# Kernel optimization log

Measured on AMD Instinct MI355X. Metric: run time of the kernel, lower is better.

## Reference

```python
import jax, jax.numpy as jnp
import numpy as np

D_K = 64

def setup_inputs() -> dict:
    key = jax.random.key(0)
    kq, kk, kv = jax.random.split(key, 3)
    shape = (2, 16, 2048, D_K)  # [B, H, S, d_k]
    q = jax.random.normal(kq, shape, dtype=jnp.float32)
    k = jax.random.normal(kk, shape, dtype=jnp.float32)
    v = jax.random.normal(kv, shape, dtype=jnp.float32)
    return {"q": q, "k": k, "v": v}

def reference(q, k, v):
    # score = q @ k^T / sqrt(d_k)  -> [B, H, S, S]
    scale = 1.0 / np.sqrt(D_K).astype(np.float32)
    score = jnp.einsum("bhqd,bhkd->bhqk", q, k) * scale
    attn = jax.nn.softmax(score, axis=-1)
    # dropout is identity in eval mode
    out = jnp.einsum("bhqk,bhkd->bhqd", attn, v)
    return out
```

## Files before the change

### kernel.cpp

```cpp
#include <hip/hip_runtime.h>
#include <hip/hip_bf16.h>
#include <math.h>
#include <stdint.h>


#define S_LEN 2048
#define DK 64
#define QW 32
#define NW 4
#define QBLK (QW * NW)
#define KVBLK 64
#define NT (S_LEN / KVBLK)
#define LOG2E 1.44269504088896340736f
#define THR 8.0f

typedef __attribute__((ext_vector_type(16))) float f32x16;
typedef __attribute__((ext_vector_type(8)))  __bf16 bf16x8;
typedef __attribute__((ext_vector_type(4)))  __bf16 bf16x4;
typedef __attribute__((ext_vector_type(4)))  uint32_t u32x4;

union frag_cast { u32x4 u; bf16x8 h; };

__device__ __forceinline__ uint32_t cvt_pk_bf16(float lo, float hi) {
    uint32_t r;
    asm("v_cvt_pk_bf16_f32 %0, %1, %2" : "=v"(r) : "v"(lo), "v"(hi));
    return r;
}
__device__ __forceinline__ void perm32swap(uint32_t& a, uint32_t& b) {
    asm volatile("v_permlane32_swap_b32 %0, %1" : "+v"(a), "+v"(b));
}
__device__ __forceinline__ void load_lds16(const __bf16* g, __bf16* l) {
    __builtin_amdgcn_global_load_lds(
        (const __attribute__((address_space(1))) void*)g,
        (__attribute__((address_space(3))) void*)l, 16, 0, 0);
}
__device__ __forceinline__ bf16x8 pack8(float4 a, float4 b) {
    bf16x8 f;
    f[0] = (__bf16)a.x; f[1] = (__bf16)a.y; f[2] = (__bf16)a.z; f[3] = (__bf16)a.w;
    f[4] = (__bf16)b.x; f[5] = (__bf16)b.y; f[6] = (__bf16)b.z; f[7] = (__bf16)b.w;
    return f;
}

__global__ __launch_bounds__(256)
void prep_pack(const float* __restrict__ Kg, const float* __restrict__ Vg,
               __bf16* __restrict__ Kimg, __bf16* __restrict__ Vimg)
{
    __shared__ float Vs[64 * 65];
    const int tid = threadIdx.x;
    const int t = blockIdx.x, bh = blockIdx.y;
    const size_t ibase = ((size_t)bh * S_LEN + (size_t)t * 64) * DK;
    const size_t obase = ((size_t)bh * NT + t) * 4096;

    #pragma unroll
    for (int u0 = 0; u0 < 2; ++u0) {
        const int u = tid + 256 * u0;
        const int f = u >> 6, lane = u & 63;
        const int sp = f >> 1, kt2 = f & 1;
        const int row = kt2 * 32 + (lane & 31);
        const int col = 16 * sp + 8 * (lane >> 5);
        const float* src = Kg + ibase + row * 64 + col;
        float4 a = *(const float4*)(src);
        float4 b = *(const float4*)(src + 4);
        *(bf16x8*)(Kimg + obase + (size_t)u * 8) = pack8(a, b);
    }

    {
        const int r = tid >> 2, c0 = (tid & 3) * 16;
        const float* src = Vg + ibase + r * 64 + c0;
        #pragma unroll
        for (int m = 0; m < 4; ++m) {
            float4 x = *(const float4*)(src + 4 * m);
            float* dst = &Vs[r * 65 + c0 + 4 * m];
            dst[0] = x.x; dst[1] = x.y; dst[2] = x.z; dst[3] = x.w;
        }
    }
    __syncthreads();
    #pragma unroll
    for (int u0 = 0; u0 < 2; ++u0) {
        const int u = tid + 256 * u0;
        const int g = u >> 6, lane = u & 63;
        const int ks = g >> 1, dt = g & 1;
        const int k0 = 16 * ks + 8 * (lane >> 5);
        const int d  = dt * 32 + (lane & 31);
        bf16x8 wv;
        #pragma unroll
        for (int i = 0; i < 8; ++i) wv[i] = (__bf16)Vs[(k0 + i) * 65 + d];
        *(bf16x8*)(Vimg + obase + (size_t)u * 8) = wv;
    }
}

__global__ __launch_bounds__(256, 2)
void attn_fwd_lds(const float* __restrict__ Qg, const __bf16* __restrict__ Kimg,
                  const __bf16* __restrict__ Vimg, float* __restrict__ Og)
{
    __shared__ __align__(16) __bf16 Kl[2][4096];
    __shared__ __align__(16) __bf16 Vt[2][4096];

    const int tid = threadIdx.x;
    const int lane = tid & 63;
    const int w   = tid >> 6;
    const int l31 = lane & 31;
    const int hi  = lane >> 5;

    const int qt = blockIdx.x;
    const int bh = blockIdx.y;
    const size_t base = (size_t)bh * (S_LEN * DK);
    const int q0g = qt * QBLK + w * QW;

    bf16x8 qf[4];
    {
        const float sc = 0.125f * LOG2E;
        const float* qrow = Qg + base + (size_t)(q0g + l31) * DK;
        #pragma unroll
        for (int sp = 0; sp < 4; ++sp) {
            const int d0 = 16 * sp + 8 * hi;
            float4 a = *(const float4*)(qrow + d0);
            float4 b = *(const float4*)(qrow + d0 + 4);
            bf16x8 f;
            f[0] = (__bf16)(a.x * sc); f[1] = (__bf16)(a.y * sc);
            f[2] = (__bf16)(a.z * sc); f[3] = (__bf16)(a.w * sc);
            f[4] = (__bf16)(b.x * sc); f[5] = (__bf16)(b.y * sc);
            f[6] = (__bf16)(b.z * sc); f[7] = (__bf16)(b.w * sc);
            qf[sp] = f;
        }
    }

    bf16x8 ones;
    #pragma unroll
    for (int i = 0; i < 8; ++i) ones[i] = (__bf16)1.0f;

    f32x16 acc0 = {}, acc1 = {}, acc2 = {};
    float m_run = -INFINITY;

    const __bf16* kbase = Kimg + (size_t)bh * NT * 4096;
    const __bf16* vbase = Vimg + (size_t)bh * NT * 4096;
    const int loff = lane * 8;

    auto stage = [&](int t, int b) {
        const __bf16* kt = kbase + (size_t)t * 4096 + tid * 8;
        const __bf16* vt = vbase + (size_t)t * 4096 + tid * 8;
        load_lds16(kt,        &Kl[b][w * 512]);
        load_lds16(kt + 2048, &Kl[b][2048 + w * 512]);
        load_lds16(vt,        &Vt[b][w * 512]);
        load_lds16(vt + 2048, &Vt[b][2048 + w * 512]);
    };

    stage(0, 0);
    __syncthreads();

    int cur = 0;
    #pragma unroll 1
    for (int t = 0; t < NT; ++t) {
        if (t + 1 < NT) stage(t + 1, cur ^ 1);

        f32x16 s0 = {}, s1 = {};
        __builtin_amdgcn_s_setprio(1);
        #pragma unroll
        for (int sp = 0; sp < 4; ++sp) {
            bf16x8 kb0 = *(const bf16x8*)(&Kl[cur][(sp * 2 + 0) * 512 + loff]);
            bf16x8 kb1 = *(const bf16x8*)(&Kl[cur][(sp * 2 + 1) * 512 + loff]);
            s0 = __builtin_amdgcn_mfma_f32_32x32x16_bf16(kb0, qf[sp], s0, 0, 0, 0);
            s1 = __builtin_amdgcn_mfma_f32_32x32x16_bf16(kb1, qf[sp], s1, 0, 0, 0);
        }
        __builtin_amdgcn_s_setprio(0);

        float a16[16];
        #pragma unroll
        for (int j = 0; j < 16; ++j) a16[j] = fmaxf(s0[j], s1[j]);
        float vmax = fmaxf(fmaxf(a16[0], a16[1]), a16[2]);
        #pragma unroll
        for (int j = 0; j < 6; ++j)
            vmax = fmaxf(fmaxf(vmax, a16[3 + 2 * j]), a16[4 + 2 * j]);
        vmax = fmaxf(vmax, a16[15]);
        vmax = fmaxf(vmax, __shfl_xor(vmax, 32));

        if (!__all(vmax - m_run <= THR)) {
            const float mnew = fmaxf(m_run, vmax);
            const float alpha = __builtin_amdgcn_exp2f(m_run - mnew);
            m_run = mnew;
            #pragma unroll
            for (int r = 0; r < 16; ++r) {
                const int ql = (r & 3) + 8 * (r >> 2) + 4 * hi;
                const float ar = __shfl(alpha, ql + (hi << 5));
                acc0[r] *= ar;
                acc1[r] *= ar;
                acc2[r] *= ar;
            }
        }

        #pragma unroll
        for (int j = 0; j < 16; ++j) s0[j] = __builtin_amdgcn_exp2f(s0[j] - m_run);
        #pragma unroll
        for (int j = 0; j < 16; ++j) s1[j] = __builtin_amdgcn_exp2f(s1[j] - m_run);

        frag_cast pa[4];
        #pragma unroll
        for (int b2 = 0; b2 < 2; ++b2) {
            #pragma unroll
            for (int st = 0; st < 2; ++st) {
                uint32_t wa, wb, wc, wd;
                if (b2 == 0) {
                    wa = cvt_pk_bf16(s0[8 * st + 0], s0[8 * st + 1]);
                    wb = cvt_pk_bf16(s0[8 * st + 2], s0[8 * st + 3]);
                    wc = cvt_pk_bf16(s0[8 * st + 4], s0[8 * st + 5]);
                    wd = cvt_pk_bf16(s0[8 * st + 6], s0[8 * st + 7]);
                } else {
                    wa = cvt_pk_bf16(s1[8 * st + 0], s1[8 * st + 1]);
                    wb = cvt_pk_bf16(s1[8 * st + 2], s1[8 * st + 3]);
                    wc = cvt_pk_bf16(s1[8 * st + 4], s1[8 * st + 5]);
                    wd = cvt_pk_bf16(s1[8 * st + 6], s1[8 * st + 7]);
                }
                perm32swap(wa, wc);
                perm32swap(wb, wd);
                pa[2 * b2 + st].u = (u32x4){wa, wb, wc, wd};
            }
        }

        __builtin_amdgcn_s_setprio(1);
        #pragma unroll
        for (int ks = 0; ks < 4; ++ks) {
            bf16x8 vb0 = *(const bf16x8*)(&Vt[cur][(ks * 2 + 0) * 512 + loff]);
            bf16x8 vb1 = *(const bf16x8*)(&Vt[cur][(ks * 2 + 1) * 512 + loff]);
            acc0 = __builtin_amdgcn_mfma_f32_32x32x16_bf16(pa[ks].h, vb0, acc0, 0, 0, 0);
            acc1 = __builtin_amdgcn_mfma_f32_32x32x16_bf16(pa[ks].h, vb1, acc1, 0, 0, 0);
            acc2 = __builtin_amdgcn_mfma_f32_32x32x16_bf16(pa[ks].h, ones, acc2, 0, 0, 0);
        }
        __builtin_amdgcn_s_setprio(0);

        __syncthreads();
        cur ^= 1;
    }

    float* op = Og + base;
    #pragma unroll
    for (int r = 0; r < 16; ++r) {
        const int ql = (r & 3) + 8 * (r >> 2) + 4 * hi;
        const float invl = 1.0f / acc2[r];
        const size_t row = (size_t)(q0g + ql) * DK;
        op[row + l31]      = acc0[r] * invl;
        op[row + 32 + l31] = acc1[r] * invl;
    }
}

__global__ __launch_bounds__(256, 2)
void attn_fwd_fb(const float* __restrict__ Qg, const float* __restrict__ Kg,
                 const float* __restrict__ Vg, float* __restrict__ Og)
{
    __shared__ __align__(16) __bf16 Kl[2][64 * 64];
    __shared__ __align__(16) __bf16 Vt[2][64 * 64];

    const int tid = threadIdx.x;
    const int lane = tid & 63;
    const int w   = tid >> 6;
    const int l31 = lane & 31;
    const int hi  = lane >> 5;

    const int qt = blockIdx.x;
    const int bh = blockIdx.y;
    const size_t base = (size_t)bh * (S_LEN * DK);
    const int q0g = qt * QBLK + w * QW;

    bf16x8 qf[4];
    {
        const float sc = 0.125f * LOG2E;
        const float* qrow = Qg + base + (size_t)(q0g + l31) * DK;
        #pragma unroll
        for (int sp = 0; sp < 4; ++sp) {
            const int d0 = 16 * sp + 8 * hi;
            float4 a = *(const float4*)(qrow + d0);
            float4 b = *(const float4*)(qrow + d0 + 4);
            bf16x8 f;
            f[0] = (__bf16)(a.x * sc); f[1] = (__bf16)(a.y * sc);
            f[2] = (__bf16)(a.z * sc); f[3] = (__bf16)(a.w * sc);
            f[4] = (__bf16)(b.x * sc); f[5] = (__bf16)(b.y * sc);
            f[6] = (__bf16)(b.z * sc); f[7] = (__bf16)(b.w * sc);
            qf[sp] = f;
        }
    }

    f32x16 acc0 = {}, acc1 = {};
    float m_run = -INFINITY, l_run = 0.f;

    float4 kpre[4];
    float  vpre[4][4];
    const int vd  = tid & 63;
    const int vkq = tid >> 6;

    auto issueLoads = [&](int t) {
        const int kv0 = t * KVBLK;
        #pragma unroll
        for (int i = 0; i < 4; ++i) {
            const int idx = tid + 256 * i;
            const int r = idx >> 4, c = idx & 15;
            kpre[i] = *(const float4*)(Kg + base + (size_t)(kv0 + r) * DK + c * 4);
        }
        #pragma unroll
        for (int i = 0; i < 4; ++i) {
            const int k0 = vkq * 4 + 16 * i;
            const float* vp = Vg + base + (size_t)(kv0 + k0) * DK + vd;
            vpre[i][0] = vp[0];      vpre[i][1] = vp[DK];
            vpre[i][2] = vp[2 * DK]; vpre[i][3] = vp[3 * DK];
        }
    };
    auto writeTile = [&](int b) {
        #pragma unroll
        for (int i = 0; i < 4; ++i) {
            const int idx = tid + 256 * i;
            const int r = idx >> 4, c = idx & 15;
            bf16x4 pk;
            pk[0] = (__bf16)kpre[i].x; pk[1] = (__bf16)kpre[i].y;
            pk[2] = (__bf16)kpre[i].z; pk[3] = (__bf16)kpre[i].w;
            *(bf16x4*)(&Kl[b][r * 64 + ((c * 4) ^ ((r & 7) << 3))]) = pk;
        }
        #pragma unroll
        for (int i = 0; i < 4; ++i) {
            const int k0 = vkq * 4 + 16 * i;
            bf16x4 pv;
            pv[0] = (__bf16)vpre[i][0]; pv[1] = (__bf16)vpre[i][1];
            pv[2] = (__bf16)vpre[i][2]; pv[3] = (__bf16)vpre[i][3];
            *(bf16x4*)(&Vt[b][vd * 64 + (k0 ^ ((vd & 7) << 3))]) = pv;
        }
    };

    issueLoads(0);
    writeTile(0);
    __syncthreads();

    int cur = 0;
    #pragma unroll 1
    for (int t = 0; t < NT; ++t) {
        if (t + 1 < NT) issueLoads(t + 1);

        f32x16 s0 = {}, s1 = {};
        __builtin_amdgcn_s_setprio(1);
        #pragma unroll
        for (int sp = 0; sp < 4; ++sp) {
            #pragma unroll
            for (int kt2 = 0; kt2 < 2; ++kt2) {
                const int krow = kt2 * 32 + l31;
                const int eo = krow * 64 + ((16 * sp + 8 * hi) ^ ((krow & 7) << 3));
                bf16x8 kb = *(const bf16x8*)(&Kl[cur][eo]);
                if (kt2 == 0) s0 = __builtin_amdgcn_mfma_f32_32x32x16_bf16(kb, qf[sp], s0, 0, 0, 0);
                else          s1 = __builtin_amdgcn_mfma_f32_32x32x16_bf16(kb, qf[sp], s1, 0, 0, 0);
            }
        }
        __builtin_amdgcn_s_setprio(0);

        float vmax = -INFINITY;
        #pragma unroll
        for (int j = 0; j < 16; ++j) vmax = fmaxf(vmax, s0[j]);
        #pragma unroll
        for (int j = 0; j < 16; ++j) vmax = fmaxf(vmax, s1[j]);
        vmax = fmaxf(vmax, __shfl_xor(vmax, 32));

        if (!__all(vmax - m_run <= THR)) {
            const float mnew = fmaxf(m_run, vmax);
            const float alpha = __builtin_amdgcn_exp2f(m_run - mnew);
            m_run = mnew;
            l_run *= alpha;
            #pragma unroll
            for (int r = 0; r < 16; ++r) {
                const int ql = (r & 3) + 8 * (r >> 2) + 4 * hi;
                const float ar = __shfl(alpha, ql + (hi << 5));
                acc0[r] *= ar;
                acc1[r] *= ar;
            }
        }

        float rs = 0.f;
        #pragma unroll
        for (int j = 0; j < 16; ++j) { const float p = __builtin_amdgcn_exp2f(s0[j] - m_run); s0[j] = p; rs += p; }
        #pragma unroll
        for (int j = 0; j < 16; ++j) { const float p = __builtin_amdgcn_exp2f(s1[j] - m_run); s1[j] = p; rs += p; }
        rs += __shfl_xor(rs, 32);
        l_run += rs;

        frag_cast pa[4];
        #pragma unroll
        for (int b2 = 0; b2 < 2; ++b2) {
            #pragma unroll
            for (int st = 0; st < 2; ++st) {
                uint32_t wa, wb, wc, wd;
                if (b2 == 0) {
                    wa = cvt_pk_bf16(s0[8 * st + 0], s0[8 * st + 1]);
                    wb = cvt_pk_bf16(s0[8 * st + 2], s0[8 * st + 3]);
                    wc = cvt_pk_bf16(s0[8 * st + 4], s0[8 * st + 5]);
                    wd = cvt_pk_bf16(s0[8 * st + 6], s0[8 * st + 7]);
                } else {
                    wa = cvt_pk_bf16(s1[8 * st + 0], s1[8 * st + 1]);
                    wb = cvt_pk_bf16(s1[8 * st + 2], s1[8 * st + 3]);
                    wc = cvt_pk_bf16(s1[8 * st + 4], s1[8 * st + 5]);
                    wd = cvt_pk_bf16(s1[8 * st + 6], s1[8 * st + 7]);
                }
                perm32swap(wa, wc);
                perm32swap(wb, wd);
                pa[2 * b2 + st].u = (u32x4){wa, wb, wc, wd};
            }
        }

        __builtin_amdgcn_s_setprio(1);
        #pragma unroll
        for (int ks = 0; ks < 4; ++ks) {
            #pragma unroll
            for (int dt = 0; dt < 2; ++dt) {
                const int d = dt * 32 + l31;
                const int eo = d * 64 + ((16 * ks + 8 * hi) ^ ((d & 7) << 3));
                bf16x8 vb = *(const bf16x8*)(&Vt[cur][eo]);
                if (dt == 0) acc0 = __builtin_amdgcn_mfma_f32_32x32x16_bf16(pa[ks].h, vb, acc0, 0, 0, 0);
                else         acc1 = __builtin_amdgcn_mfma_f32_32x32x16_bf16(pa[ks].h, vb, acc1, 0, 0, 0);
            }
        }
        __builtin_amdgcn_s_setprio(0);

        if (t + 1 < NT) writeTile(cur ^ 1);
        __syncthreads();
        cur ^= 1;
    }

    float* op = Og + base;
    #pragma unroll
    for (int r = 0; r < 16; ++r) {
        const int ql = (r & 3) + 8 * (r >> 2) + 4 * hi;
        const float lr = __shfl(l_run, ql + (hi << 5));
        const float invl = 1.0f / lr;
        const size_t row = (size_t)(q0g + ql) * DK;
        op[row + l31]      = acc0[r] * invl;
        op[row + 32 + l31] = acc1[r] * invl;
    }
}

extern "C" void kernel_launch(void* const* d_in, const int* in_sizes, int n_in,
                              void* d_out, int out_size, void* d_ws, size_t ws_size,
                              hipStream_t stream) {
    const float* q = (const float*)d_in[0];
    const float* k = (const float*)d_in[1];
    const float* v = (const float*)d_in[2];
    float* o = (float*)d_out;
    const int bh = in_sizes[0] / (S_LEN * DK);

    const size_t img_bytes = (size_t)bh * NT * 4096 * sizeof(__bf16);
    if (ws_size >= 2 * img_bytes) {
        __bf16* Kimg = (__bf16*)d_ws;
        __bf16* Vimg = (__bf16*)((char*)d_ws + img_bytes);
        prep_pack<<<dim3(NT, bh), dim3(256), 0, stream>>>(k, v, Kimg, Vimg);
        attn_fwd_lds<<<dim3(S_LEN / QBLK, bh), dim3(256), 0, stream>>>(q, Kimg, Vimg, o);
    } else {
        attn_fwd_fb<<<dim3(S_LEN / QBLK, bh), dim3(256), 0, stream>>>(q, k, v, o);
    }
}
```

Baseline: 68.24 us.

## Triple-buffer K/V LDS tiles with vmcnt waits and XCD-aware block remap

The LDS path moves from double to triple buffering. Each tile is prefetched two iterations ahead, and the full __syncthreads is replaced with s_waitcnt vmcnt plus a raw s_barrier, so global-to-LDS loads overlap more compute. Blocks are also remapped so that the query tiles of a given batch-head land on the same XCD, which should improve L2 reuse of K/V. LDS use per block rises by half, which may limit occupancy, and the fallback kernel loses its setprio hints.

```diff
diff --git a/kernel.cpp b/kernel.cpp
--- a/kernel.cpp
+++ b/kernel.cpp
@@ -93,8 +93,8 @@
 void attn_fwd_lds(const float* __restrict__ Qg, const __bf16* __restrict__ Kimg,
                   const __bf16* __restrict__ Vimg, float* __restrict__ Og)
 {
-    __shared__ __align__(16) __bf16 Kl[2][4096];
-    __shared__ __align__(16) __bf16 Vt[2][4096];
+    __shared__ __align__(16) __bf16 Kl[3][4096];
+    __shared__ __align__(16) __bf16 Vt[3][4096];
 
     const int tid = threadIdx.x;
     const int lane = tid & 63;
@@ -102,8 +102,16 @@
     const int l31 = lane & 31;
     const int hi  = lane >> 5;
 
-    const int qt = blockIdx.x;
-    const int bh = blockIdx.y;
+    int qt, bh;
+    {
+        const int lin = blockIdx.y * gridDim.x + blockIdx.x;
+        if (gridDim.x * gridDim.y == 512) {
+            const int xcd = lin & 7, slot = lin >> 3;
+            bh = xcd * 4 + (slot >> 4);
+            qt = slot & 15;
+        } else { qt = blockIdx.x; bh = blockIdx.y; }
+    }
+
     const size_t base = (size_t)bh * (S_LEN * DK);
     const int q0g = qt * QBLK + w * QW;
 
@@ -146,12 +154,15 @@
     };
 
     stage(0, 0);
-    __syncthreads();
-
-    int cur = 0;
+    stage(1, 1);
+    asm volatile("s_waitcnt vmcnt(4)" ::: "memory");
+    __builtin_amdgcn_s_barrier();
+    __builtin_amdgcn_sched_barrier(0);
+
+    int cur = 0, nxt = 1, nn = 2;
     #pragma unroll 1
     for (int t = 0; t < NT; ++t) {
-        if (t + 1 < NT) stage(t + 1, cur ^ 1);
+        if (t + 2 < NT) stage(t + 2, nn);
 
         f32x16 s0 = {}, s1 = {};
         __builtin_amdgcn_s_setprio(1);
@@ -227,8 +238,16 @@
         }
         __builtin_amdgcn_s_setprio(0);
 
-        __syncthreads();
-        cur ^= 1;
+        if (t + 2 < NT) {
+            asm volatile("s_waitcnt vmcnt(4)" ::: "memory");
+        } else if (t + 1 < NT) {
+            asm volatile("s_waitcnt vmcnt(0)" ::: "memory");
+        }
+        if (t + 1 < NT) {
+            __builtin_amdgcn_s_barrier();
+            __builtin_amdgcn_sched_barrier(0);
+        }
+        const int tmp = cur; cur = nxt; nxt = nn; nn = tmp;
     }
 
     float* op = Og + base;
@@ -332,7 +351,6 @@
         if (t + 1 < NT) issueLoads(t + 1);
 
         f32x16 s0 = {}, s1 = {};
-        __builtin_amdgcn_s_setprio(1);
         #pragma unroll
         for (int sp = 0; sp < 4; ++sp) {
             #pragma unroll
@@ -344,7 +362,6 @@
                 else          s1 = __builtin_amdgcn_mfma_f32_32x32x16_bf16(kb, qf[sp], s1, 0, 0, 0);
             }
         }
-        __builtin_amdgcn_s_setprio(0);
 
         float vmax = -INFINITY;
         #pragma unroll
@@ -398,7 +415,6 @@
             }
         }
 
-        __builtin_amdgcn_s_setprio(1);
         #pragma unroll
         for (int ks = 0; ks < 4; ++ks) {
             #pragma unroll
@@ -410,7 +426,6 @@
                 else         acc1 = __builtin_amdgcn_mfma_f32_32x32x16_bf16(pa[ks].h, vb, acc1, 0, 0, 0);
             }
         }
-        __builtin_amdgcn_s_setprio(0);
 
         if (t + 1 < NT) writeTile(cur ^ 1);
         __syncthreads();
```

Measured after the change: 68.78 us. About the same (+0.8%).
